# Kernel optimization log

Measured on AMD Instinct MI355X. Metric: run time of the kernel, lower is better.

## Reference

```python
import jax, jax.numpy as jnp
import numpy as np

B, N, F_IN = 4, 4096, 64
N_DIM, N_PROP, N_FILT = 4, 64, 128
K_NEIGH = 40
EXP_FACTOR = 10.0


def setup_inputs() -> dict:
    key = jax.random.key(0)
    ks = jax.random.split(key, 4)
    x = jax.random.normal(ks[0], (B, N, F_IN), dtype=jnp.float32)
    W_flr = jax.random.normal(ks[1], (F_IN, N_PROP), dtype=jnp.float32) * (1.0 / np.sqrt(F_IN))
    b_flr = jnp.zeros((N_PROP,), jnp.float32)
    W_s = jax.random.normal(ks[2], (F_IN, N_DIM), dtype=jnp.float32) * (1.0 / np.sqrt(F_IN))
    b_s = jnp.zeros((N_DIM,), jnp.float32)
    W_out = jax.random.normal(ks[3], (F_IN + 2 * N_PROP, N_FILT), dtype=jnp.float32) * (1.0 / np.sqrt(F_IN + 2 * N_PROP))
    b_out = jnp.zeros((N_FILT,), jnp.float32)
    return {"x": x, "W_flr": W_flr, "b_flr": b_flr, "W_s": W_s, "b_s": b_s, "W_out": W_out, "b_out": b_out}


def _euclidean_squared(A):
    # [B,N,D] -> [B,N,N] squared euclidean distance (abs for numerical safety)
    sub = -2.0 * jnp.einsum("bnd,bmd->bnm", A, A)
    dot = jnp.sum(A * A, axis=2)
    return jnp.abs(sub + dot[:, :, None] + dot[:, None, :])


def reference(x, W_flr, b_flr, W_s, b_s, W_out, b_out):
    features = x @ W_flr + b_flr                 # [B,N,P]
    coordinates = x @ W_s + b_s                  # [B,N,D]
    dist = _euclidean_squared(coordinates)       # [B,N,N]
    # top_k of -dist => nearest neighbours (first is self)
    ranked_neg, ranked_idx = jax.lax.top_k(-dist, K_NEIGH)
    nbr_idx = ranked_idx[:, :, 1:]               # [B,N,K-1]
    distance = -ranked_neg[:, :, 1:]             # positive distances
    weights = jnp.exp(-jnp.abs(distance * EXP_FACTOR))[..., None]  # [B,N,K-1,1]
    # gather neighbour features per batch: [B,N,K-1,P]
    nbr_feats = jax.vmap(lambda f, i: f[i])(features, nbr_idx) * weights
    agg = jnp.concatenate([jnp.max(nbr_feats, axis=2), jnp.mean(nbr_feats, axis=2)], axis=-1)
    updated = jnp.concatenate([x, agg], axis=-1)  # [B,N,F_IN+2P]
    return updated @ W_out + b_out               # [B,N,n_filters]
```

## Files before the change

kernel.cpp:

```cpp
#include <hip/hip_runtime.h>
#include <hip/hip_bf16.h>
#include <stdint.h>

#define B_    4
#define N_    4096
#define FIN   64
#define NPROP 64
#define NFILT 128
#define KSEL  40
#define ROWS  (B_ * N_)
#define CAP   160
#define CAPP  176

typedef __attribute__((ext_vector_type(8)))  short short8;
typedef __attribute__((ext_vector_type(4)))  float f32x4;
typedef __attribute__((ext_vector_type(16))) float f32x16;

__device__ __forceinline__ unsigned b16rne(float v) {
    unsigned u = __float_as_uint(v);
    return (u + 0x7FFFu + ((u >> 16) & 1u)) >> 16;
}
__device__ __forceinline__ float fromb16(unsigned h) {
    return __uint_as_float(h << 16);
}
__device__ __forceinline__ unsigned neg2pk(unsigned p) {
    return (p + 0x00800080u) ^ 0x80008000u;
}
__device__ __forceinline__ uint2 pk4(unsigned a, unsigned b, unsigned c, unsigned d) {
    return make_uint2(a | (b << 16), c | (d << 16));
}

__global__ __launch_bounds__(192) void k0_packW(
    const float* __restrict__ Wo, unsigned short* __restrict__ Wpk)
{
    int c = blockIdx.x, k = threadIdx.x;
    float wv = Wo[k * NFILT + c];
    unsigned wh = b16rne(wv);
    unsigned wl = b16rne(wv - fromb16(wh));
    Wpk[(size_t)c * 576 + k]       = (unsigned short)wh;
    Wpk[(size_t)c * 576 + 192 + k] = (unsigned short)wh;
    Wpk[(size_t)c * 576 + 384 + k] = (unsigned short)wl;
}

__global__ __launch_bounds__(256) void k1_proj(
    const float* __restrict__ x, const float* __restrict__ Wf, const float* __restrict__ bf,
    const float* __restrict__ Ws, const float* __restrict__ bs,
    float* __restrict__ feat, uint4* __restrict__ Bpk)
{
    int wid  = threadIdx.x >> 6;
    int lane = threadIdx.x & 63;
    int base = blockIdx.x * 16 + wid * 4;

    float xv[4], ac[4];
    float4 cr[4];
    float4 bs4 = make_float4(bs[0], bs[1], bs[2], bs[3]);
    float bfl = bf[lane];
    #pragma unroll
    for (int r = 0; r < 4; ++r) {
        xv[r] = x[(size_t)(base + r) * FIN + lane];
        ac[r] = bfl;
        cr[r] = bs4;
    }
    #pragma unroll 16
    for (int k = 0; k < FIN; ++k) {
        float wf = Wf[k * NPROP + lane];
        float4 w4 = reinterpret_cast<const float4*>(Ws)[k];
        #pragma unroll
        for (int r = 0; r < 4; ++r) {
            float xk = __shfl(xv[r], k);
            ac[r] = fmaf(xk, wf, ac[r]);
            cr[r].x = fmaf(xk, w4.x, cr[r].x);
            cr[r].y = fmaf(xk, w4.y, cr[r].y);
            cr[r].z = fmaf(xk, w4.z, cr[r].z);
            cr[r].w = fmaf(xk, w4.w, cr[r].w);
        }
    }
    #pragma unroll
    for (int r = 0; r < 4; ++r)
        feat[(size_t)(base + r) * NPROP + lane] = ac[r];

    #pragma unroll
    for (int r = 0; r < 4; ++r) {
        float c0 = cr[r].x, c1 = cr[r].y, c2 = cr[r].z, c3 = cr[r].w;
        unsigned h0 = b16rne(c0), h1 = b16rne(c1), h2 = b16rne(c2), h3 = b16rne(c3);
        unsigned l0 = b16rne(c0 - fromb16(h0)), l1 = b16rne(c1 - fromb16(h1));
        unsigned l2 = b16rne(c2 - fromb16(h2)), l3 = b16rne(c3 - fromb16(h3));
        float n = c0 * c0; n = fmaf(c1, c1, n); n = fmaf(c2, c2, n); n = fmaf(c3, c3, n);
        unsigned nih = b16rne(n), nil = b16rne(n - fromb16(nih));
        unsigned v0 = h0 | (h1 << 16), v1 = h2 | (h3 << 16);
        unsigned v4 = l0 | (l1 << 16), v5 = l2 | (l3 << 16);
        unsigned on2 = 0x3F803F80u, nn = nih | (nil << 16);
        if (lane < 2) {
            uint4 p = lane ? make_uint4(v4, v5, on2, nn) : make_uint4(v0, v1, v0, v1);
            Bpk[(size_t)(base + r) * 2 + lane] = p;
        }
    }
}

__global__ __launch_bounds__(1024, 8) void k2_knn(
    const uint4* __restrict__ Bpk, const float* __restrict__ feat,
    const float* __restrict__ x, const unsigned short* __restrict__ Wpk,
    const float* __restrict__ bo, float* __restrict__ out)
{
    __shared__ unsigned minlds[32][132];
    __shared__ unsigned survK[32][CAPP];
    __shared__ unsigned taulds[32];
    __shared__ int      cnt[32];
    __shared__ unsigned winC[32][KSEL];
    __shared__ unsigned short Upk[32][392];

    int tid = threadIdx.x, w = tid >> 6, lane = tid & 63;
    int strip = blockIdx.x & 127;
    int b     = blockIdx.x >> 7;
    int q0    = strip * 32;
    int col = lane & 31, h = lane >> 5;
    int g = lane >> 4, li = lane & 15;
    size_t pbase = (size_t)b * N_;

    if (tid < 32) cnt[tid] = 0;

    short8 afr;
    {
        uint4 u0 = Bpk[(pbase + q0 + col) * 2 + 0];
        uint4 u1 = Bpk[(pbase + q0 + col) * 2 + 1];
        union { uint4 u; short8 s; } cv;
        cv.u = (h == 0) ? make_uint4(neg2pk(u0.x), neg2pk(u0.y), neg2pk(u1.x), neg2pk(u1.y))
                        : make_uint4(neg2pk(u0.x), neg2pk(u0.y), u1.w, u1.z);
        afr = cv.s;
    }

    const uint4* bp = Bpk + (pbase + w * 256 + col) * 2 + h;

    float fm[16];
    #pragma unroll
    for (int r = 0; r < 16; ++r) fm[r] = 1e30f;
    uint4 nb = bp[0];
    #pragma unroll
    for (int t = 0; t < 8; ++t) {
        union { uint4 u; short8 s; } bv; bv.u = nb;
        if (t < 7) nb = bp[(t + 1) * 64];
        f32x16 d = __builtin_amdgcn_mfma_f32_32x32x16_bf16(afr, bv.s, (f32x16){0.f}, 0, 0, 0);
        #pragma unroll
        for (int r = 0; r < 16; ++r) fm[r] = fminf(fm[r], d[r]);
    }
    #pragma unroll
    for (int r = 0; r < 16; ++r) {
        float v = fm[r];
        v = fminf(v, __shfl_xor(v, 8));
        v = fminf(v, __shfl_xor(v, 16));
        fm[r] = v;
    }
    if ((lane & 24) == 0) {
        #pragma unroll
        for (int r = 0; r < 16; ++r) {
            int row = (r & 3) + 8 * (r >> 2) + 4 * h;
            minlds[row][w * 8 + (lane & 7)] = __float_as_uint(fmaxf(fm[r], 0.0f));
        }
    }
    __syncthreads();

    unsigned sv[2];
    #pragma unroll
    for (int e = 0; e < 2; ++e) {
        int r = 2 * w + e;
        sv[e] = min(minlds[r][lane], minlds[r][64 + lane]);
    }
    #pragma unroll
    for (int k = 2; k <= 64; k <<= 1) {
        #pragma unroll
        for (int j2 = k >> 1; j2 >= 1; j2 >>= 1) {
            bool up = (((lane & k) == 0) == ((lane & j2) == 0));
            #pragma unroll
            for (int e = 0; e < 2; ++e) {
                unsigned o = (unsigned)__shfl_xor((int)sv[e], j2);
                sv[e] = up ? min(sv[e], o) : max(sv[e], o);
            }
        }
    }
    if (lane == 39) {
        taulds[2 * w]     = (sv[0] & 0xFFFFF000u) | 0xFFFu;
        taulds[2 * w + 1] = (sv[1] & 0xFFFFF000u) | 0xFFFu;
    }
    __syncthreads();

    float tauF[16];
    #pragma unroll
    for (int r = 0; r < 16; ++r)
        tauF[r] = __uint_as_float(taulds[(r & 3) + 8 * (r >> 2) + 4 * h]);

    bool selfDiag = (h == ((col >> 2) & 1));
    int  rs       = ((col >> 3) << 2) | (col & 3);
    int  tdiag    = (w == (strip >> 3)) ? (strip & 7) : 99;

    nb = bp[0];
    #pragma unroll 2
    for (int t = 0; t < 8; ++t) {
        union { uint4 u; short8 s; } bv; bv.u = nb;
        if (t < 7) nb = bp[(t + 1) * 64];
        f32x16 d = __builtin_amdgcn_mfma_f32_32x32x16_bf16(afr, bv.s, (f32x16){0.f}, 0, 0, 0);
        unsigned idx = (unsigned)((w * 8 + t) * 32 + col);
        if (t == tdiag) {
            #pragma unroll
            for (int r = 0; r < 16; ++r) {
                int rowc = (r & 3) + 8 * (r >> 2) + 4 * h;
                if (selfDiag && r == rs) {
                    int s = atomicAdd(&cnt[rowc], 1); if (s < CAP) survK[rowc][s] = 0u;
                } else if (d[r] <= tauF[r]) {
                    unsigned c = (__float_as_uint(fmaxf(d[r], 0.f)) & 0xFFFFF000u) | idx;
                    int s = atomicAdd(&cnt[rowc], 1); if (s < CAP) survK[rowc][s] = c;
                }
            }
        } else {
            #pragma unroll
            for (int r = 0; r < 16; ++r) {
                if (d[r] <= tauF[r]) {
                    int rowc = (r & 3) + 8 * (r >> 2) + 4 * h;
                    unsigned c = (__float_as_uint(fmaxf(d[r], 0.f)) & 0xFFFFF000u) | idx;
                    int s = atomicAdd(&cnt[rowc], 1); if (s < CAP) survK[rowc][s] = c;
                }
            }
        }
    }
    __syncthreads();

    #pragma unroll
    for (int e = 0; e < 2; ++e) {
        int r = 2 * w + e;
        int S = min(cnt[r], CAP);
        if (lane < 16) survK[r][S + lane] = 0xFFFFFFFFu;
        for (int rr = lane; rr < S; rr += 64) {
            unsigned my = survK[r][rr];
            int c = 0;
            int S4 = (S + 3) >> 2;
            for (int s4 = 0; s4 < S4; ++s4) {
                uint4 u4 = *reinterpret_cast<const uint4*>(&survK[r][4 * s4]);
                c += (u4.x < my) + (u4.y < my) + (u4.z < my) + (u4.w < my);
            }
            if (c >= 1 && c < KSEL) winC[r][c - 1] = my;
        }
    }

    #pragma unroll
    for (int e = 0; e < 2; ++e) {
        int r = 2 * w + e;
        float xv = x[(pbase + q0 + r) * FIN + lane];
        unsigned xh = b16rne(xv), xl = b16rne(xv - fromb16(xh));
        Upk[r][lane]       = (unsigned short)xh;
        Upk[r][192 + lane] = (unsigned short)xl;
    }

    {
        int l15 = lane & 15;
        int gi  = (lane >> 4) & 1;
        int rw  = 2 * w + (lane >> 5);
        const float4* fr = reinterpret_cast<const float4*>(feat + pbase * NPROP);
        float4 mx4 = make_float4(-3.4e38f, -3.4e38f, -3.4e38f, -3.4e38f);
        float4 sm4 = make_float4(0.f, 0.f, 0.f, 0.f);
        #pragma unroll 4
        for (int i = 0; i < 20; ++i) {
            int n = gi * 20 + i;
            if (n < KSEL - 1) {
                unsigned comp = winC[rw][n];
                int j = (int)(comp & 0xFFFu);
                float dd = __uint_as_float(comp & 0xFFFFF000u);
                float wt = __expf(-10.f * dd);
                float4 f4 = fr[j * 16 + l15];
                float wx = wt * f4.x, wy = wt * f4.y, wz = wt * f4.z, ww = wt * f4.w;
                mx4.x = fmaxf(mx4.x, wx); sm4.x += wx;
                mx4.y = fmaxf(mx4.y, wy); sm4.y += wy;
                mx4.z = fmaxf(mx4.z, wz); sm4.z += wz;
                mx4.w = fmaxf(mx4.w, ww); sm4.w += ww;
            }
        }
        mx4.x = fmaxf(mx4.x, __shfl_xor(mx4.x, 16)); sm4.x += __shfl_xor(sm4.x, 16);
        mx4.y = fmaxf(mx4.y, __shfl_xor(mx4.y, 16)); sm4.y += __shfl_xor(sm4.y, 16);
        mx4.z = fmaxf(mx4.z, __shfl_xor(mx4.z, 16)); sm4.z += __shfl_xor(sm4.z, 16);
        mx4.w = fmaxf(mx4.w, __shfl_xor(mx4.w, 16)); sm4.w += __shfl_xor(sm4.w, 16);

        if (gi == 0) {
            unsigned h0 = b16rne(mx4.x), h1 = b16rne(mx4.y), h2 = b16rne(mx4.z), h3 = b16rne(mx4.w);
            unsigned o0 = b16rne(mx4.x - fromb16(h0)), o1 = b16rne(mx4.y - fromb16(h1));
            unsigned o2 = b16rne(mx4.z - fromb16(h2)), o3 = b16rne(mx4.w - fromb16(h3));
            *reinterpret_cast<uint2*>(&Upk[rw][64  + 4 * l15]) = pk4(h0, h1, h2, h3);
            *reinterpret_cast<uint2*>(&Upk[rw][256 + 4 * l15]) = pk4(o0, o1, o2, o3);
        } else {
            float ex = sm4.x * (1.0f / 39.0f), ey = sm4.y * (1.0f / 39.0f);
            float ez = sm4.z * (1.0f / 39.0f), ew = sm4.w * (1.0f / 39.0f);
            unsigned h0 = b16rne(ex), h1 = b16rne(ey), h2 = b16rne(ez), h3 = b16rne(ew);
            unsigned o0 = b16rne(ex - fromb16(h0)), o1 = b16rne(ey - fromb16(h1));
            unsigned o2 = b16rne(ez - fromb16(h2)), o3 = b16rne(ew - fromb16(h3));
            *reinterpret_cast<uint2*>(&Upk[rw][128 + 4 * l15]) = pk4(h0, h1, h2, h3);
            *reinterpret_cast<uint2*>(&Upk[rw][320 + 4 * l15]) = pk4(o0, o1, o2, o3);
        }
    }
    __syncthreads();

    {
        int rh   = w >> 3;
        int colc = (w & 7) * 16 + li;
        const unsigned short* wp = Wpk + (size_t)colc * 576;
        f32x4 oacc = {0.f, 0.f, 0.f, 0.f};
        #pragma unroll
        for (int s = 0; s < 18; ++s) {
            int koff = (s < 6)  ? (32 * s + 8 * g)
                     : (s < 12) ? (192 + 32 * (s - 6) + 8 * g)
                                : (32 * (s - 12) + 8 * g);
            union { uint4 u; short8 s8; } av, bv;
            av.u = *reinterpret_cast<const uint4*>(&Upk[rh * 16 + li][koff]);
            bv.u = *reinterpret_cast<const uint4*>(&wp[32 * s + 8 * g]);
            oacc = __builtin_amdgcn_mfma_f32_16x16x32_bf16(av.s8, bv.s8, oacc, 0, 0, 0);
        }
        float bb = bo[colc];
        #pragma unroll
        for (int e = 0; e < 4; ++e) {
            int orow = rh * 16 + g * 4 + e;
            out[(size_t)(pbase + q0 + orow) * NFILT + colc] = oacc[e] + bb;
        }
    }
}

extern "C" void kernel_launch(void* const* d_in, const int* in_sizes, int n_in,
                              void* d_out, int out_size, void* d_ws, size_t ws_size,
                              hipStream_t stream)
{
    const float* x  = (const float*)d_in[0];
    const float* Wf = (const float*)d_in[1];
    const float* bf = (const float*)d_in[2];
    const float* Ws = (const float*)d_in[3];
    const float* bs = (const float*)d_in[4];
    const float* Wo = (const float*)d_in[5];
    const float* bo = (const float*)d_in[6];
    float* out = (float*)d_out;

    float*          feat = (float*)d_ws;
    uint4*          Bpk  = (uint4*)((char*)d_ws + (size_t)ROWS * NPROP * 4);
    unsigned short* Wpk  = (unsigned short*)((char*)d_ws
                             + (size_t)ROWS * NPROP * 4 + (size_t)ROWS * 32);

    k0_packW<<<NFILT, 192, 0, stream>>>(Wo, Wpk);
    k1_proj <<<ROWS / 16, 256, 0, stream>>>(x, Wf, bf, Ws, bs, feat, Bpk);
    k2_knn  <<<B_ * 128, 1024, 0, stream>>>(Bpk, feat, x, Wpk, bo, out);
}
```

Measured before the change: 83.88 us.

## Compute input projections with split-bf16 MFMA instead of scalar FMA

The feature and coordinate projections in k1_proj now run on bf16 MFMA. Inputs and weights are split into hi/lo bf16 parts and combined with three products, which keeps close to fp32 accuracy. The weights are pre-packed into MFMA fragment layout inside the extended k0 kernel, and each block now handles 64 rows instead of 16. This targets the shuffle-heavy scalar FMA loop in the projection stage. The cost is extra packing work, an LDS round trip for the coordinates, and a small precision change in the projected values.

```diff
diff --git a/kernel.cpp b/kernel.cpp
--- a/kernel.cpp
+++ b/kernel.cpp
@@ -30,58 +30,138 @@
     return make_uint2(a | (b << 16), c | (d << 16));
 }
 
-__global__ __launch_bounds__(192) void k0_packW(
-    const float* __restrict__ Wo, unsigned short* __restrict__ Wpk)
+__global__ __launch_bounds__(192) void k0_pack(
+    const float* __restrict__ Wo, const float* __restrict__ Wf,
+    const float* __restrict__ Ws, unsigned short* __restrict__ Wpk,
+    uint4* __restrict__ Wfpk, uint4* __restrict__ Wspk)
 {
-    int c = blockIdx.x, k = threadIdx.x;
-    float wv = Wo[k * NFILT + c];
-    unsigned wh = b16rne(wv);
-    unsigned wl = b16rne(wv - fromb16(wh));
-    Wpk[(size_t)c * 576 + k]       = (unsigned short)wh;
-    Wpk[(size_t)c * 576 + 192 + k] = (unsigned short)wh;
-    Wpk[(size_t)c * 576 + 384 + k] = (unsigned short)wl;
+    int blk = blockIdx.x, tid = threadIdx.x;
+    if (blk < 128) {
+        int c = blk, k = tid;
+        float wv = Wo[k * NFILT + c];
+        unsigned wh = b16rne(wv);
+        unsigned wl = b16rne(wv - fromb16(wh));
+        Wpk[(size_t)c * 576 + k]       = (unsigned short)wh;
+        Wpk[(size_t)c * 576 + 192 + k] = (unsigned short)wh;
+        Wpk[(size_t)c * 576 + 384 + k] = (unsigned short)wl;
+    } else if (blk < 132) {
+        int ct = blk - 128;
+        for (int idx = tid; idx < 256; idx += 192) {
+            int q = idx >> 6, l = idx & 63, c = l & 15, g = l >> 4;
+            int kb = (q & 1) * 32 + 8 * g;
+            bool hi = (q < 2);
+            unsigned u[4];
+            #pragma unroll
+            for (int p = 0; p < 4; ++p) {
+                float v0 = Wf[(kb + 2 * p) * NPROP + ct * 16 + c];
+                float v1 = Wf[(kb + 2 * p + 1) * NPROP + ct * 16 + c];
+                unsigned h0 = b16rne(v0), h1 = b16rne(v1);
+                unsigned e0 = hi ? h0 : b16rne(v0 - fromb16(h0));
+                unsigned e1 = hi ? h1 : b16rne(v1 - fromb16(h1));
+                u[p] = e0 | (e1 << 16);
+            }
+            Wfpk[ct * 256 + idx] = make_uint4(u[0], u[1], u[2], u[3]);
+        }
+    } else {
+        for (int idx = tid; idx < 256; idx += 192) {
+            int q = idx >> 6, l = idx & 63, c = l & 15, g = l >> 4;
+            int kb = (q & 1) * 32 + 8 * g;
+            bool hi = (q < 2);
+            unsigned u[4];
+            #pragma unroll
+            for (int p = 0; p < 4; ++p) {
+                float v0 = (c < 4) ? Ws[(kb + 2 * p) * 4 + c] : 0.f;
+                float v1 = (c < 4) ? Ws[(kb + 2 * p + 1) * 4 + c] : 0.f;
+                unsigned h0 = b16rne(v0), h1 = b16rne(v1);
+                unsigned e0 = hi ? h0 : b16rne(v0 - fromb16(h0));
+                unsigned e1 = hi ? h1 : b16rne(v1 - fromb16(h1));
+                u[p] = e0 | (e1 << 16);
+            }
+            Wspk[idx] = make_uint4(u[0], u[1], u[2], u[3]);
+        }
+    }
 }
 
 __global__ __launch_bounds__(256) void k1_proj(
-    const float* __restrict__ x, const float* __restrict__ Wf, const float* __restrict__ bf,
-    const float* __restrict__ Ws, const float* __restrict__ bs,
-    float* __restrict__ feat, uint4* __restrict__ Bpk)
+    const float* __restrict__ x, const uint4* __restrict__ Wfpk,
+    const uint4* __restrict__ Wspk, const float* __restrict__ bf,
+    const float* __restrict__ bs, float* __restrict__ feat,
+    uint4* __restrict__ Bpk)
 {
-    int wid  = threadIdx.x >> 6;
-    int lane = threadIdx.x & 63;
-    int base = blockIdx.x * 16 + wid * 4;
-
-    float xv[4], ac[4];
-    float4 cr[4];
-    float4 bs4 = make_float4(bs[0], bs[1], bs[2], bs[3]);
-    float bfl = bf[lane];
-    #pragma unroll
-    for (int r = 0; r < 4; ++r) {
-        xv[r] = x[(size_t)(base + r) * FIN + lane];
-        ac[r] = bfl;
-        cr[r] = bs4;
-    }
-    #pragma unroll 16
-    for (int k = 0; k < FIN; ++k) {
-        float wf = Wf[k * NPROP + lane];
-        float4 w4 = reinterpret_cast<const float4*>(Ws)[k];
-        #pragma unroll
-        for (int r = 0; r < 4; ++r) {
-            float xk = __shfl(xv[r], k);
-            ac[r] = fmaf(xk, wf, ac[r]);
-            cr[r].x = fmaf(xk, w4.x, cr[r].x);
-            cr[r].y = fmaf(xk, w4.y, cr[r].y);
-            cr[r].z = fmaf(xk, w4.z, cr[r].z);
-            cr[r].w = fmaf(xk, w4.w, cr[r].w);
-        }
-    }
-    #pragma unroll
-    for (int r = 0; r < 4; ++r)
-        feat[(size_t)(base + r) * NPROP + lane] = ac[r];
-
-    #pragma unroll
-    for (int r = 0; r < 4; ++r) {
-        float c0 = cr[r].x, c1 = cr[r].y, c2 = cr[r].z, c3 = cr[r].w;
+    __shared__ float clds[4][16][20];
+    int wv = threadIdx.x >> 6, lane = threadIdx.x & 63;
+    int li = lane & 15, g = lane >> 4;
+    int rbase = blockIdx.x * 64 + wv * 16;
+
+    const float* xr = x + (size_t)(rbase + li) * FIN + 8 * g;
+    float4 a0 = *reinterpret_cast<const float4*>(xr);
+    float4 a1 = *reinterpret_cast<const float4*>(xr + 4);
+    float4 b0 = *reinterpret_cast<const float4*>(xr + 32);
+    float4 b1 = *reinterpret_cast<const float4*>(xr + 36);
+
+    float av[8] = {a0.x, a0.y, a0.z, a0.w, a1.x, a1.y, a1.z, a1.w};
+    float bv[8] = {b0.x, b0.y, b0.z, b0.w, b1.x, b1.y, b1.z, b1.w};
+    unsigned xh01u[4], xl01u[4], xh23u[4], xl23u[4];
+    #pragma unroll
+    for (int p = 0; p < 4; ++p) {
+        unsigned h0 = b16rne(av[2 * p]), h1 = b16rne(av[2 * p + 1]);
+        xh01u[p] = h0 | (h1 << 16);
+        xl01u[p] = b16rne(av[2 * p] - fromb16(h0)) | (b16rne(av[2 * p + 1] - fromb16(h1)) << 16);
+        unsigned g0 = b16rne(bv[2 * p]), g1 = b16rne(bv[2 * p + 1]);
+        xh23u[p] = g0 | (g1 << 16);
+        xl23u[p] = b16rne(bv[2 * p] - fromb16(g0)) | (b16rne(bv[2 * p + 1] - fromb16(g1)) << 16);
+    }
+    union { uint4 u; short8 s; } XH01, XL01, XH23, XL23;
+    XH01.u = make_uint4(xh01u[0], xh01u[1], xh01u[2], xh01u[3]);
+    XL01.u = make_uint4(xl01u[0], xl01u[1], xl01u[2], xl01u[3]);
+    XH23.u = make_uint4(xh23u[0], xh23u[1], xh23u[2], xh23u[3]);
+    XL23.u = make_uint4(xl23u[0], xl23u[1], xl23u[2], xl23u[3]);
+
+    #pragma unroll
+    for (int ct = 0; ct < 4; ++ct) {
+        union { uint4 u; short8 s; } wh01, wh23, wl01, wl23;
+        wh01.u = Wfpk[ct * 256 + 0 * 64 + lane];
+        wh23.u = Wfpk[ct * 256 + 1 * 64 + lane];
+        wl01.u = Wfpk[ct * 256 + 2 * 64 + lane];
+        wl23.u = Wfpk[ct * 256 + 3 * 64 + lane];
+        float bfv = bf[ct * 16 + li];
+        f32x4 acc = {bfv, bfv, bfv, bfv};
+        acc = __builtin_amdgcn_mfma_f32_16x16x32_bf16(XH01.s, wh01.s, acc, 0, 0, 0);
+        acc = __builtin_amdgcn_mfma_f32_16x16x32_bf16(XH23.s, wh23.s, acc, 0, 0, 0);
+        acc = __builtin_amdgcn_mfma_f32_16x16x32_bf16(XL01.s, wh01.s, acc, 0, 0, 0);
+        acc = __builtin_amdgcn_mfma_f32_16x16x32_bf16(XL23.s, wh23.s, acc, 0, 0, 0);
+        acc = __builtin_amdgcn_mfma_f32_16x16x32_bf16(XH01.s, wl01.s, acc, 0, 0, 0);
+        acc = __builtin_amdgcn_mfma_f32_16x16x32_bf16(XH23.s, wl23.s, acc, 0, 0, 0);
+        #pragma unroll
+        for (int e = 0; e < 4; ++e)
+            feat[(size_t)(rbase + g * 4 + e) * NPROP + ct * 16 + li] = acc[e];
+    }
+
+    {
+        union { uint4 u; short8 s; } wh01, wh23, wl01, wl23;
+        wh01.u = Wspk[0 * 64 + lane];
+        wh23.u = Wspk[1 * 64 + lane];
+        wl01.u = Wspk[2 * 64 + lane];
+        wl23.u = Wspk[3 * 64 + lane];
+        float bsv = (li < 4) ? bs[li] : 0.f;
+        f32x4 acc = {bsv, bsv, bsv, bsv};
+        acc = __builtin_amdgcn_mfma_f32_16x16x32_bf16(XH01.s, wh01.s, acc, 0, 0, 0);
+        acc = __builtin_amdgcn_mfma_f32_16x16x32_bf16(XH23.s, wh23.s, acc, 0, 0, 0);
+        acc = __builtin_amdgcn_mfma_f32_16x16x32_bf16(XL01.s, wh01.s, acc, 0, 0, 0);
+        acc = __builtin_amdgcn_mfma_f32_16x16x32_bf16(XL23.s, wh23.s, acc, 0, 0, 0);
+        acc = __builtin_amdgcn_mfma_f32_16x16x32_bf16(XH01.s, wl01.s, acc, 0, 0, 0);
+        acc = __builtin_amdgcn_mfma_f32_16x16x32_bf16(XH23.s, wl23.s, acc, 0, 0, 0);
+        if (li < 4) {
+            #pragma unroll
+            for (int e = 0; e < 4; ++e) clds[wv][g * 4 + e][li] = acc[e];
+        }
+    }
+    __syncthreads();
+
+    if (lane < 16) {
+        int row = rbase + lane;
+        float c0 = clds[wv][lane][0], c1 = clds[wv][lane][1];
+        float c2 = clds[wv][lane][2], c3 = clds[wv][lane][3];
         unsigned h0 = b16rne(c0), h1 = b16rne(c1), h2 = b16rne(c2), h3 = b16rne(c3);
         unsigned l0 = b16rne(c0 - fromb16(h0)), l1 = b16rne(c1 - fromb16(h1));
         unsigned l2 = b16rne(c2 - fromb16(h2)), l3 = b16rne(c3 - fromb16(h3));
@@ -89,11 +169,8 @@
         unsigned nih = b16rne(n), nil = b16rne(n - fromb16(nih));
         unsigned v0 = h0 | (h1 << 16), v1 = h2 | (h3 << 16);
         unsigned v4 = l0 | (l1 << 16), v5 = l2 | (l3 << 16);
-        unsigned on2 = 0x3F803F80u, nn = nih | (nil << 16);
-        if (lane < 2) {
-            uint4 p = lane ? make_uint4(v4, v5, on2, nn) : make_uint4(v0, v1, v0, v1);
-            Bpk[(size_t)(base + r) * 2 + lane] = p;
-        }
+        Bpk[(size_t)row * 2 + 0] = make_uint4(v0, v1, v0, v1);
+        Bpk[(size_t)row * 2 + 1] = make_uint4(v4, v5, 0x3F803F80u, nih | (nil << 16));
     }
 }
 
@@ -137,9 +214,9 @@
     uint4 nb = bp[0];
     #pragma unroll
     for (int t = 0; t < 8; ++t) {
-        union { uint4 u; short8 s; } bv; bv.u = nb;
+        union { uint4 u; short8 s; } bvv; bvv.u = nb;
         if (t < 7) nb = bp[(t + 1) * 64];
-        f32x16 d = __builtin_amdgcn_mfma_f32_32x32x16_bf16(afr, bv.s, (f32x16){0.f}, 0, 0, 0);
+        f32x16 d = __builtin_amdgcn_mfma_f32_32x32x16_bf16(afr, bvv.s, (f32x16){0.f}, 0, 0, 0);
         #pragma unroll
         for (int r = 0; r < 16; ++r) fm[r] = fminf(fm[r], d[r]);
     }
@@ -195,9 +272,9 @@
     nb = bp[0];
     #pragma unroll 2
     for (int t = 0; t < 8; ++t) {
-        union { uint4 u; short8 s; } bv; bv.u = nb;
+        union { uint4 u; short8 s; } bvv; bvv.u = nb;
         if (t < 7) nb = bp[(t + 1) * 64];
-        f32x16 d = __builtin_amdgcn_mfma_f32_32x32x16_bf16(afr, bv.s, (f32x16){0.f}, 0, 0, 0);
+        f32x16 d = __builtin_amdgcn_mfma_f32_32x32x16_bf16(afr, bvv.s, (f32x16){0.f}, 0, 0, 0);
         unsigned idx = (unsigned)((w * 8 + t) * 32 + col);
         if (t == tdiag) {
             #pragma unroll
@@ -305,10 +382,10 @@
             int koff = (s < 6)  ? (32 * s + 8 * g)
                      : (s < 12) ? (192 + 32 * (s - 6) + 8 * g)
                                 : (32 * (s - 12) + 8 * g);
-            union { uint4 u; short8 s8; } av, bv;
-            av.u = *reinterpret_cast<const uint4*>(&Upk[rh * 16 + li][koff]);
-            bv.u = *reinterpret_cast<const uint4*>(&wp[32 * s + 8 * g]);
-            oacc = __builtin_amdgcn_mfma_f32_16x16x32_bf16(av.s8, bv.s8, oacc, 0, 0, 0);
+            union { uint4 u; short8 s8; } av, bvv;
+            av.u  = *reinterpret_cast<const uint4*>(&Upk[rh * 16 + li][koff]);
+            bvv.u = *reinterpret_cast<const uint4*>(&wp[32 * s + 8 * g]);
+            oacc = __builtin_amdgcn_mfma_f32_16x16x32_bf16(av.s8, bvv.s8, oacc, 0, 0, 0);
         }
         float bb = bo[colc];
         #pragma unroll
@@ -332,12 +409,16 @@
     const float* bo = (const float*)d_in[6];
     float* out = (float*)d_out;
 
-    float*          feat = (float*)d_ws;
-    uint4*          Bpk  = (uint4*)((char*)d_ws + (size_t)ROWS * NPROP * 4);
-    unsigned short* Wpk  = (unsigned short*)((char*)d_ws
-                             + (size_t)ROWS * NPROP * 4 + (size_t)ROWS * 32);
-
-    k0_packW<<<NFILT, 192, 0, stream>>>(Wo, Wpk);
-    k1_proj <<<ROWS / 16, 256, 0, stream>>>(x, Wf, bf, Ws, bs, feat, Bpk);
-    k2_knn  <<<B_ * 128, 1024, 0, stream>>>(Bpk, feat, x, Wpk, bo, out);
-}
+    char* wsb = (char*)d_ws;
+    float*          feat = (float*)wsb;
+    uint4*          Bpk  = (uint4*)(wsb + (size_t)ROWS * NPROP * 4);
+    unsigned short* Wpk  = (unsigned short*)(wsb + (size_t)ROWS * NPROP * 4
+                                                 + (size_t)ROWS * 32);
+    uint4* Wfpk = (uint4*)(wsb + (size_t)ROWS * NPROP * 4 + (size_t)ROWS * 32
+                               + 147456);
+    uint4* Wspk = Wfpk + 1024;
+
+    k0_pack<<<133, 192, 0, stream>>>(Wo, Wf, Ws, Wpk, Wfpk, Wspk);
+    k1_proj<<<ROWS / 64, 256, 0, stream>>>(x, Wfpk, Wspk, bf, bs, feat, Bpk);
+    k2_knn <<<B_ * 128, 1024, 0, stream>>>(Bpk, feat, x, Wpk, bo, out);
+}
```

Result: faster. 72.23 us (-13.9%).
